# Kernel tuning notes

Measured on AMD Instinct MI355X. Metric: run time of the kernel, lower is better.

## Reference

```python
import jax, jax.numpy as jnp
import numpy as np

EPS = 1e-8  # torch CosineSimilarity default eps


def setup_inputs() -> dict:
    key = jax.random.key(0)
    k1, k2, k3 = jax.random.split(key, 3)
    B, H, Lq, Lc, D = 8, 16, 128, 4096, 1024
    return {
        "question_emb": jax.random.normal(k1, (B, Lq, D), dtype=jnp.float32),
        "context_emb": jax.random.normal(k2, (B, Lc, D), dtype=jnp.float32),
        "cross_attn_weights": jax.random.uniform(k3, (B, H, Lq, Lc), dtype=jnp.float32),
    }


def reference(question_emb, context_emb, cross_attn_weights, topk: int = 5):
    # avg attention over heads and query tokens -> [B, Lc]
    avg_attn = cross_attn_weights.mean(axis=(1, 2))
    k = min(topk, context_emb.shape[1])
    _, idx = jax.lax.top_k(avg_attn, k)  # idx: [B, k]
    # gather top-k context vectors: [B, k, D]
    top_ctx = jnp.take_along_axis(context_emb, idx[:, :, None], axis=1)
    # mean question vector per batch: [B, D]
    q_vec = question_emb.mean(axis=1)
    # cosine similarity with torch-style eps clamping on each norm
    q_norm = jnp.maximum(jnp.linalg.norm(q_vec, axis=-1, keepdims=True), EPS)  # [B,1]
    c_norm = jnp.maximum(jnp.linalg.norm(top_ctx, axis=-1), EPS)               # [B,k]
    dots = jnp.einsum("bd,bkd->bk", q_vec, top_ctx)
    sim = dots / (q_norm * c_norm)  # [B, k]
    # per-batch mean of (1 - sim), then mean over batch (k is constant -> global mean)
    return (1.0 - sim).mean()
```

## Files before the change

### kernel.cpp

```cpp
#include <hip/hip_runtime.h>
#include <math.h>

#define BB 8
#define HH 16
#define LQ 128
#define LC 4096
#define DD 1024
#define ROWS (HH * LQ)
#define R_SLABS 32
#define ROWS_PER_SLAB (ROWS / R_SLABS)
#define COL_TILES 4
#define K1_BLOCKS (BB * COL_TILES * R_SLABS)
#define QV_BLOCKS ((BB * DD) / 256)
#define KTOP 5
#define EPSF 1e-8f

__global__ __launch_bounds__(256) void kA_partials_qv(
    const float* __restrict__ attn, const float* __restrict__ q,
    float* __restrict__ partials, float* __restrict__ qv,
    float* __restrict__ out) {
    if (blockIdx.x == 0 && threadIdx.x == 0) *out = 0.0f;

    int blk = blockIdx.x;
    if (blk < K1_BLOCKS) {
        int r = blk % R_SLABS;
        int t = blk / R_SLABS;
        int ct = t % COL_TILES;
        int b = t / COL_TILES;
        int col = ct * 1024 + threadIdx.x * 4;

        const float4* src = (const float4*)(attn + (size_t)b * ROWS * LC
                                                 + (size_t)r * ROWS_PER_SLAB * LC + col);
        float4 acc = make_float4(0.f, 0.f, 0.f, 0.f);
#pragma unroll 8
        for (int m = 0; m < ROWS_PER_SLAB; ++m) {
            float4 v = src[(size_t)m * (LC / 4)];
            acc.x += v.x; acc.y += v.y; acc.z += v.z; acc.w += v.w;
        }
        float4* dst = (float4*)(partials + (size_t)r * BB * LC + (size_t)b * LC + col);
        *dst = acc;
    } else {
        int g = (blk - K1_BLOCKS) * 256 + threadIdx.x;
        int b = g / DD;
        int d = g % DD;
        const float* p = q + (size_t)b * LQ * DD + d;
        float s = 0.f;
#pragma unroll 8
        for (int row = 0; row < LQ; ++row)
            s += p[(size_t)row * DD];
        qv[g] = s * (1.0f / LQ);
    }
}

__global__ __launch_bounds__(1024) void kB_topk_finalize(
    const float* __restrict__ partials, const float* __restrict__ qv,
    const float* __restrict__ ctx, float* __restrict__ out) {
    __shared__ float swv[16];
    __shared__ int   swi[16];
    __shared__ int   s_win;
    __shared__ int   s_top[KTOP];
    __shared__ float sred[4][11];

    int b = blockIdx.x;
    int tid = threadIdx.x;
    int lane = tid & 63;
    int wave = tid >> 6;

    float v[4] = {0.f, 0.f, 0.f, 0.f};
    const float* pb = partials + (size_t)b * LC + (size_t)tid * 4;
#pragma unroll
    for (int r = 0; r < R_SLABS; ++r) {
        float4 p = *(const float4*)(pb + (size_t)r * BB * LC);
        v[0] += p.x; v[1] += p.y; v[2] += p.z; v[3] += p.w;
    }

    for (int kk = 0; kk < KTOP; ++kk) {
        float bv = v[0];
        int bj = 0;
#pragma unroll
        for (int j = 1; j < 4; ++j)
            if (v[j] > bv) { bv = v[j]; bj = j; }
        int bc = tid * 4 + bj;

        for (int off = 32; off > 0; off >>= 1) {
            float ov = __shfl_down(bv, off);
            int   oc = __shfl_down(bc, off);
            if (ov > bv || (ov == bv && oc < bc)) { bv = ov; bc = oc; }
        }
        if (lane == 0) { swv[wave] = bv; swi[wave] = bc; }
        __syncthreads();
        if (tid == 0) {
            float fv = swv[0]; int fc = swi[0];
#pragma unroll
            for (int w = 1; w < 16; ++w)
                if (swv[w] > fv || (swv[w] == fv && swi[w] < fc)) { fv = swv[w]; fc = swi[w]; }
            s_top[kk] = fc;
            s_win = fc;
        }
        __syncthreads();
        int wc = s_win;
        if ((wc >> 2) == tid) v[wc & 3] = -3.0e38f;
    }

    if (tid < 256) {
        const float4 q4 = *((const float4*)(qv + (size_t)b * DD + tid * 4));
        float acc[11];
        acc[10] = q4.x * q4.x + q4.y * q4.y + q4.z * q4.z + q4.w * q4.w;
#pragma unroll
        for (int kk = 0; kk < KTOP; ++kk) {
            const float4 c4 = *((const float4*)(ctx + (size_t)b * LC * DD
                                                + (size_t)s_top[kk] * DD + tid * 4));
            acc[kk]     = q4.x * c4.x + q4.y * c4.y + q4.z * c4.z + q4.w * c4.w;
            acc[5 + kk] = c4.x * c4.x + c4.y * c4.y + c4.z * c4.z + c4.w * c4.w;
        }
        for (int off = 32; off > 0; off >>= 1) {
#pragma unroll
            for (int i = 0; i < 11; ++i)
                acc[i] += __shfl_down(acc[i], off);
        }
        if (lane == 0) {
#pragma unroll
            for (int i = 0; i < 11; ++i) sred[wave][i] = acc[i];
        }
    }
    __syncthreads();
    if (tid == 0) {
        float t[11];
#pragma unroll
        for (int i = 0; i < 11; ++i)
            t[i] = sred[0][i] + sred[1][i] + sred[2][i] + sred[3][i];
        float qn = fmaxf(sqrtf(t[10]), EPSF);
        float loss = 0.f;
#pragma unroll
        for (int kk = 0; kk < KTOP; ++kk) {
            float cn = fmaxf(sqrtf(t[5 + kk]), EPSF);
            loss += 1.0f - t[kk] / (qn * cn);
        }
        atomicAdd(out, loss * (1.0f / (BB * KTOP)));
    }
}

extern "C" void kernel_launch(void* const* d_in, const int* in_sizes, int n_in,
                              void* d_out, int out_size, void* d_ws, size_t ws_size,
                              hipStream_t stream) {
    const float* q    = (const float*)d_in[0];
    const float* ctx  = (const float*)d_in[1];
    const float* attn = (const float*)d_in[2];
    float* out = (float*)d_out;

    float* partials = (float*)d_ws;
    float* qv = partials + (size_t)R_SLABS * BB * LC;

    kA_partials_qv<<<K1_BLOCKS + QV_BLOCKS, 256, 0, stream>>>(attn, q, partials, qv, out);
    kB_topk_finalize<<<BB, 1024, 0, stream>>>(partials, qv, ctx, out);
}
```

Measured before the change: 427.1 us.

## Split top-k stage into per-slice blocks with last-block candidate merge

```diff
diff --git a/kernel.cpp b/kernel.cpp
--- a/kernel.cpp
+++ b/kernel.cpp
@@ -12,19 +12,24 @@
 #define COL_TILES 4
 #define K1_BLOCKS (BB * COL_TILES * R_SLABS)
 #define QV_BLOCKS ((BB * DD) / 256)
+#define SLICES 4
 #define KTOP 5
 #define EPSF 1e-8f
 
 __global__ __launch_bounds__(256) void kA_partials_qv(
     const float* __restrict__ attn, const float* __restrict__ q,
     float* __restrict__ partials, float* __restrict__ qv,
-    float* __restrict__ out) {
-    if (blockIdx.x == 0 && threadIdx.x == 0) *out = 0.0f;
+    unsigned int* __restrict__ done, float* __restrict__ out) {
+    if (blockIdx.x == 0) {
+        if (threadIdx.x < BB) done[threadIdx.x] = 0u;
+        if (threadIdx.x == BB) *out = 0.0f;
+    }
 
     int blk = blockIdx.x;
-    if (blk < K1_BLOCKS) {
-        int r = blk % R_SLABS;
-        int t = blk / R_SLABS;
+    if (blk >= QV_BLOCKS) {
+        int kblk = blk - QV_BLOCKS;
+        int r = kblk % R_SLABS;
+        int t = kblk / R_SLABS;
         int ct = t % COL_TILES;
         int b = t / COL_TILES;
         int col = ct * 1024 + threadIdx.x * 4;
@@ -32,7 +37,7 @@
         const float4* src = (const float4*)(attn + (size_t)b * ROWS * LC
                                                  + (size_t)r * ROWS_PER_SLAB * LC + col);
         float4 acc = make_float4(0.f, 0.f, 0.f, 0.f);
-#pragma unroll 8
+#pragma unroll 16
         for (int m = 0; m < ROWS_PER_SLAB; ++m) {
             float4 v = src[(size_t)m * (LC / 4)];
             acc.x += v.x; acc.y += v.y; acc.z += v.z; acc.w += v.w;
@@ -40,7 +45,7 @@
         float4* dst = (float4*)(partials + (size_t)r * BB * LC + (size_t)b * LC + col);
         *dst = acc;
     } else {
-        int g = (blk - K1_BLOCKS) * 256 + threadIdx.x;
+        int g = blk * 256 + threadIdx.x;
         int b = g / DD;
         int d = g % DD;
         const float* p = q + (size_t)b * LQ * DD + d;
@@ -52,22 +57,30 @@
     }
 }
 
-__global__ __launch_bounds__(1024) void kB_topk_finalize(
+__global__ __launch_bounds__(256) void kB_topk_cos(
     const float* __restrict__ partials, const float* __restrict__ qv,
-    const float* __restrict__ ctx, float* __restrict__ out) {
-    __shared__ float swv[16];
-    __shared__ int   swi[16];
+    const float* __restrict__ ctx, float* __restrict__ cand_val,
+    int* __restrict__ cand_idx, unsigned int* __restrict__ done,
+    float* __restrict__ out) {
+    __shared__ float swv[4];
+    __shared__ int   swi[4];
     __shared__ int   s_win;
+    __shared__ float s_cval[KTOP];
+    __shared__ int   s_cidx[KTOP];
+    __shared__ int   s_last;
     __shared__ int   s_top[KTOP];
     __shared__ float sred[4][11];
 
-    int b = blockIdx.x;
+    int blk = blockIdx.x;
+    int b  = blk >> 2;
+    int qt = blk & 3;
     int tid = threadIdx.x;
     int lane = tid & 63;
     int wave = tid >> 6;
+    int colbase = qt * 1024 + tid * 4;
 
     float v[4] = {0.f, 0.f, 0.f, 0.f};
-    const float* pb = partials + (size_t)b * LC + (size_t)tid * 4;
+    const float* pb = partials + (size_t)b * LC + colbase;
 #pragma unroll
     for (int r = 0; r < R_SLABS; ++r) {
         float4 p = *(const float4*)(pb + (size_t)r * BB * LC);
@@ -80,7 +93,7 @@
 #pragma unroll
         for (int j = 1; j < 4; ++j)
             if (v[j] > bv) { bv = v[j]; bj = j; }
-        int bc = tid * 4 + bj;
+        int bc = colbase + bj;
 
         for (int off = 32; off > 0; off >>= 1) {
             float ov = __shfl_down(bv, off);
@@ -92,36 +105,72 @@
         if (tid == 0) {
             float fv = swv[0]; int fc = swi[0];
 #pragma unroll
-            for (int w = 1; w < 16; ++w)
+            for (int w = 1; w < 4; ++w)
                 if (swv[w] > fv || (swv[w] == fv && swi[w] < fc)) { fv = swv[w]; fc = swi[w]; }
-            s_top[kk] = fc;
+            s_cval[kk] = fv;
+            s_cidx[kk] = fc;
             s_win = fc;
         }
         __syncthreads();
-        int wc = s_win;
-        if ((wc >> 2) == tid) v[wc & 3] = -3.0e38f;
-    }
-
-    if (tid < 256) {
-        const float4 q4 = *((const float4*)(qv + (size_t)b * DD + tid * 4));
-        float acc[11];
-        acc[10] = q4.x * q4.x + q4.y * q4.y + q4.z * q4.z + q4.w * q4.w;
-#pragma unroll
+        int lcol = s_win - qt * 1024;
+        if ((lcol >> 2) == tid) v[lcol & 3] = -3.0e38f;
+    }
+
+    if (tid < KTOP) {
+        cand_val[blk * KTOP + tid] = s_cval[tid];
+        cand_idx[blk * KTOP + tid] = s_cidx[tid];
+    }
+    __syncthreads();
+    if (tid == 0) {
+        __threadfence();
+        unsigned int old = atomicAdd(&done[b], 1u);
+        s_last = (old == SLICES - 1) ? 1 : 0;
+    }
+    __syncthreads();
+    if (!s_last) return;
+
+    if (tid == 0) {
+        __threadfence();
+        float cv[SLICES * KTOP];
+        int   ci[SLICES * KTOP];
+        bool  used[SLICES * KTOP];
+#pragma unroll
+        for (int i = 0; i < SLICES * KTOP; ++i) {
+            cv[i] = cand_val[(b * SLICES) * KTOP + i];
+            ci[i] = cand_idx[(b * SLICES) * KTOP + i];
+            used[i] = false;
+        }
         for (int kk = 0; kk < KTOP; ++kk) {
-            const float4 c4 = *((const float4*)(ctx + (size_t)b * LC * DD
-                                                + (size_t)s_top[kk] * DD + tid * 4));
-            acc[kk]     = q4.x * c4.x + q4.y * c4.y + q4.z * c4.z + q4.w * c4.w;
-            acc[5 + kk] = c4.x * c4.x + c4.y * c4.y + c4.z * c4.z + c4.w * c4.w;
-        }
-        for (int off = 32; off > 0; off >>= 1) {
-#pragma unroll
-            for (int i = 0; i < 11; ++i)
-                acc[i] += __shfl_down(acc[i], off);
-        }
-        if (lane == 0) {
-#pragma unroll
-            for (int i = 0; i < 11; ++i) sred[wave][i] = acc[i];
-        }
+            int best = -1;
+            for (int i = 0; i < SLICES * KTOP; ++i) {
+                if (used[i]) continue;
+                if (best < 0 || cv[i] > cv[best] ||
+                    (cv[i] == cv[best] && ci[i] < ci[best])) best = i;
+            }
+            used[best] = true;
+            s_top[kk] = ci[best];
+        }
+    }
+    __syncthreads();
+
+    const float4 q4 = *((const float4*)(qv + (size_t)b * DD + tid * 4));
+    float acc[11];
+    acc[10] = q4.x * q4.x + q4.y * q4.y + q4.z * q4.z + q4.w * q4.w;
+#pragma unroll
+    for (int kk = 0; kk < KTOP; ++kk) {
+        const float4 c4 = *((const float4*)(ctx + (size_t)b * LC * DD
+                                            + (size_t)s_top[kk] * DD + tid * 4));
+        acc[kk]     = q4.x * c4.x + q4.y * c4.y + q4.z * c4.z + q4.w * c4.w;
+        acc[5 + kk] = c4.x * c4.x + c4.y * c4.y + c4.z * c4.z + c4.w * c4.w;
+    }
+    for (int off = 32; off > 0; off >>= 1) {
+#pragma unroll
+        for (int i = 0; i < 11; ++i)
+            acc[i] += __shfl_down(acc[i], off);
+    }
+    if (lane == 0) {
+#pragma unroll
+        for (int i = 0; i < 11; ++i) sred[wave][i] = acc[i];
     }
     __syncthreads();
     if (tid == 0) {
@@ -149,8 +198,11 @@
     float* out = (float*)d_out;
 
     float* partials = (float*)d_ws;
-    float* qv = partials + (size_t)R_SLABS * BB * LC;
-
-    kA_partials_qv<<<K1_BLOCKS + QV_BLOCKS, 256, 0, stream>>>(attn, q, partials, qv, out);
-    kB_topk_finalize<<<BB, 1024, 0, stream>>>(partials, qv, ctx, out);
+    float* qv       = partials + (size_t)R_SLABS * BB * LC;
+    float* cand_val = qv + (size_t)BB * DD;
+    int*   cand_idx = (int*)(cand_val + SLICES * BB * KTOP);
+    unsigned int* done = (unsigned int*)(cand_idx + SLICES * BB * KTOP);
+
+    kA_partials_qv<<<QV_BLOCKS + K1_BLOCKS, 256, 0, stream>>>(attn, q, partials, qv, done, out);
+    kB_topk_cos<<<BB * SLICES, 256, 0, stream>>>(partials, qv, ctx, cand_val, cand_idx, done, out);
 }
```

Result: no change. 425.8 us (-0.3%).
